# Optimization experiments

Measured on AMD Instinct MI355X. Metric: run time of the kernel, lower is better.

The kernel has to match this reference:

```python
import jax, jax.numpy as jnp
import numpy as np

CENTER = 7          # center_size
K = 5               # neighbourhood_size
DIL = 1             # dilation
EPS_LN = 1e-5       # torch F.layer_norm default eps
EPS_COS = 1e-8      # torch F.cosine_similarity default eps


def _unfold_image(image, k):
    """torch F.unfold(image, k, stride=1, padding=k//2) -> [B, T, C*k*k]."""
    B, C, H, W = image.shape
    p = k // 2
    padded = jnp.pad(image, ((0, 0), (0, 0), (p, p), (p, p)))
    # channel-major patch layout (c, ki, kj), matching torch.unfold
    patches = jnp.stack([padded[:, :, i:i + H, j:j + W]
                         for i in range(k) for j in range(k)], axis=2)  # [B,C,k*k,H,W]
    return patches.reshape(B, C * k * k, H * W).transpose(0, 2, 1)       # [B,T,D]


def _neighbour_indices(H, W, k, dil):
    """generate_local_indices with constant padding value N=H*W, center removed -> [T, k*k-1]."""
    half = (k - 1) // 2 * dil
    N = H * W
    inds = np.arange(N).reshape(H, W)
    padded = np.full((H + 2 * half, W + 2 * half), N, dtype=np.int64)
    padded[half:half + H, half:half + W] = inds
    cols = [padded[i * dil:i * dil + H, j * dil:j * dil + W].reshape(-1)
            for i in range(k) for j in range(k)]
    local = np.stack(cols, axis=-1)  # [T, k*k]
    center = (k * k) // 2
    keep = [s for s in range(k * k) if s != center]
    return jnp.asarray(local[:, keep])  # [T, S], S = k*k-1


def setup_inputs() -> dict:
    key = jax.random.key(0)
    image = jax.random.uniform(key, (2, 3, 128, 128), dtype=jnp.float32)
    return {"image": image}


def reference(image):
    B, C, H, W = image.shape
    T = H * W
    kc = CENTER

    # im2col of center patches: [B, T, C*kc*kc]
    bu = _unfold_image(image, kc)

    # per-channel LayerNorm over kc*kc elements (no affine), then +1.0 twice
    bu = bu.reshape(B, T, C, kc * kc)
    mu = bu.mean(axis=-1, keepdims=True)
    var = ((bu - mu) ** 2).mean(axis=-1, keepdims=True)
    bu = (bu - mu) / jnp.sqrt(var + EPS_LN)
    bu = bu.reshape(B, T, C * kc * kc) + 2.0  # [B,T,D]

    # local neighbourhood indices (padding index == T marks out-of-bounds)
    nb = _neighbour_indices(H, W, K, DIL)  # [T, S]

    # gather surround patches; row T is the invalid (zero) row
    bu_ext = jnp.concatenate([bu, jnp.zeros((B, 1, bu.shape[-1]), bu.dtype)], axis=1)
    surround = bu_ext[:, nb]  # [B,T,S,D]

    # cosine similarity between each center patch and its S neighbours
    dot = jnp.einsum('btd,btsd->bts', bu, surround)
    n_node = jnp.linalg.norm(bu, axis=-1)        # [B,T]
    n_sur = jnp.linalg.norm(surround, axis=-1)   # [B,T,S]
    cos = dot / jnp.maximum(n_node[:, :, None] * n_sur, EPS_COS)
    dist = (1.0 - cos) * 0.5  # = 1 - (1+cos)/2

    # masked mean over valid neighbours
    mask = (nb != T).astype(dist.dtype)  # [T,S]
    sal = (dist * mask).sum(-1) / mask.sum(-1)
    return sal.reshape(B, H, W)
```

## Files before the change

### kernel.cpp

```cpp
#include <hip/hip_runtime.h>

#define HH 128
#define WW 128
#define TX 8
#define TY 8
#define IR 22
#define ISTR 23
#define S4 16
#define S4S 17
#define S2 12
#define S2S 13
#define NTHR 256

__global__ void __launch_bounds__(NTHR)
err_kernel(const float* __restrict__ img, float* __restrict__ out) {
    __shared__ float s_img[3][IR][ISTR];
    __shared__ union U1 {
        float rs[2][3][IR][S4S];
        float H[36][18][S2];
    } u1;
    __shared__ float s_mu[3][S4][S4S];
    __shared__ float s_r [3][S4][S4S];
    __shared__ union U2 {
        float nsq[3][S2][S2S];
        float part[12][S2][S2S];
    } u2;
    __shared__ float s_rnrm[S2][S2S];

    const int tid = threadIdx.x;
    const int x0 = blockIdx.x * TX, y0 = blockIdx.y * TY;
    const float* imgb = img + (size_t)blockIdx.z * 3 * HH * WW;

    for (int i = tid; i < 3 * IR * IR; i += NTHR) {
        const int c = i / (IR * IR);
        const int rem = i - c * IR * IR;
        const int iy = rem / IR, ix = rem - iy * IR;
        const int yy = y0 - 7 + iy, xx = x0 - 7 + ix;
        float v = 0.f;
        if ((unsigned)yy < HH && (unsigned)xx < WW)
            v = imgb[c * HH * WW + yy * WW + xx];
        s_img[c][iy][ix] = v;
    }
    __syncthreads();

    if (tid < 66) {
        const int c = tid / 22, row = tid - c * 22;
        float f[22];
#pragma unroll
        for (int j = 0; j < 22; ++j) f[j] = s_img[c][row][j];
        float s = 0.f, s2 = 0.f;
#pragma unroll
        for (int k = 0; k < 7; ++k) { s += f[k]; s2 = fmaf(f[k], f[k], s2); }
        u1.rs[0][c][row][0] = s; u1.rs[1][c][row][0] = s2;
#pragma unroll
        for (int x = 1; x < S4; ++x) {
            s += f[x + 6] - f[x - 1];
            s2 += fmaf(f[x + 6], f[x + 6], -f[x - 1] * f[x - 1]);
            u1.rs[0][c][row][x] = s; u1.rs[1][c][row][x] = s2;
        }
    }
    __syncthreads();

    if (tid < 96) {
        const int c = tid / 32;
        const int rem = tid - c * 32;
        const int col = rem >> 1, h = rem & 1;
        const int r0 = h * 8;
        float s = 0.f, s2 = 0.f;
#pragma unroll
        for (int k = 0; k < 7; ++k) { s += u1.rs[0][c][r0 + k][col]; s2 += u1.rs[1][c][r0 + k][col]; }
#pragma unroll
        for (int i = 0; i < 8; ++i) {
            const int rr4 = r0 + i;
            const float mu  = s * (1.f / 49.f);
            const float var = fmaxf(fmaf(-mu, mu, s2 * (1.f / 49.f)), 0.f);
            const float rv  = rsqrtf(var + 1e-5f);
            s_mu[c][rr4][col] = mu;
            s_r [c][rr4][col] = rv;
            const int sr = rr4 - 2, sc = col - 2;
            if ((unsigned)sr < S2 && (unsigned)sc < S2)
                u2.nsq[c][sr][sc] = fmaf(49.f * var, rv * rv, 196.f);
            if (i < 7) {
                s  += u1.rs[0][c][rr4 + 7][col] - u1.rs[0][c][rr4][col];
                s2 += u1.rs[1][c][rr4 + 7][col] - u1.rs[1][c][rr4][col];
            }
        }
    }
    __syncthreads();

    if (tid < 144) {
        const int py = tid / 12, px = tid - py * 12;
        s_rnrm[py][px] = rsqrtf(u2.nsq[0][py][px] + u2.nsq[1][py][px] + u2.nsq[2][py][px]);
    }
    for (int q = tid; q < 648; q += NTHR) {
        const int cd = q / 18;
        const int prow = q - cd * 18;
        const int dI = cd / 3, c = cd - dI * 3;
        const int u = dI + 13;
        const int dy = u / 5 - 2, dx = u - (u / 5) * 5 - 2;
        const float* rowA = &s_img[c][prow + 2][2];
        const float* rowB = &s_img[c][prow + 2 + dy][2 + dx];
        float P[18];
#pragma unroll
        for (int j = 0; j < 18; ++j) P[j] = rowA[j] * rowB[j];
        float hsum = P[0] + P[1] + P[2] + P[3] + P[4] + P[5] + P[6];
        u1.H[cd][prow][0] = hsum;
#pragma unroll
        for (int j = 1; j < S2; ++j) { hsum += P[j + 6] - P[j - 1]; u1.H[cd][prow][j] = hsum; }
    }
    __syncthreads();

    if (tid < 144) {
        const int dI = tid / 12, col = tid - dI * 12;
        const int u = dI + 13;
        const int dy = u / 5 - 2, dx = u - (u / 5) * 5 - 2;
        float B[3];
#pragma unroll
        for (int c = 0; c < 3; ++c) {
            float b = 0.f;
#pragma unroll
            for (int k = 0; k < 7; ++k) b += u1.H[dI * 3 + c][k][col];
            B[c] = b;
        }
#pragma unroll
        for (int y = 0; y < S2; ++y) {
            float acc = 0.f;
#pragma unroll
            for (int c = 0; c < 3; ++c) {
                const float m = s_mu[c][y + 2][col + 2] * s_mu[c][y + 2 + dy][col + 2 + dx];
                const float v = fmaf(-49.f, m, B[c]);
                acc = fmaf(v, s_r[c][y + 2][col + 2] * s_r[c][y + 2 + dy][col + 2 + dx], acc);
            }
            u2.part[dI][y][col] = acc;
            if (y < S2 - 1) {
#pragma unroll
                for (int c = 0; c < 3; ++c)
                    B[c] += u1.H[dI * 3 + c][y + 7][col] - u1.H[dI * 3 + c][y][col];
            }
        }
    }
    __syncthreads();

    if (tid < 64) {
        const int ty = tid >> 3, tx = tid & 7;
        const int gy = y0 + ty, gx = x0 + tx;
        const float rnt = s_rnrm[ty + 2][tx + 2];
        float acc = 0.f, cnt = 0.f;
#pragma unroll
        for (int dI = 0; dI < 12; ++dI) {
            const int u = dI + 13;
            const int dy = u / 5 - 2, dx = u - (u / 5) * 5 - 2;
            if ((unsigned)(gy + dy) < HH && (unsigned)(gx + dx) < WW) {
                const float ps = u2.part[dI][ty + 2][tx + 2];
                acc = fmaf(588.f + ps, s_rnrm[ty + 2 + dy][tx + 2 + dx], acc);
                cnt += 1.f;
            }
            if ((unsigned)(gy - dy) < HH && (unsigned)(gx - dx) < WW) {
                const float ps = u2.part[dI][ty + 2 - dy][tx + 2 - dx];
                acc = fmaf(588.f + ps, s_rnrm[ty + 2 - dy][tx + 2 - dx], acc);
                cnt += 1.f;
            }
        }
        out[(size_t)blockIdx.z * HH * WW + gy * WW + gx] = 0.5f - acc * rnt / (2.f * cnt);
    }
}

extern "C" void kernel_launch(void* const* d_in, const int* in_sizes, int n_in,
                              void* d_out, int out_size, void* d_ws, size_t ws_size,
                              hipStream_t stream) {
    const float* img = (const float*)d_in[0];
    float* out = (float*)d_out;
    dim3 grid(WW / TX, HH / TY, 2);
    dim3 block(NTHR);
    hipLaunchKernelGGL(err_kernel, grid, block, 0, stream, img, out);
}
```

Measured before the change: 14.38 us.

## Vectorize shared-memory access and regroup product-row work by vertical offset

Pads the image tile row stride to 28 so rows can be read with float4 loads. Merges per-channel mean and rstd into one interleaved stat array holding rv and mu*rv, so the neighbour pass fetches them with float4 loads. The horizontal product-sum stage now assigns one thread per (dy, channel, row), reusing loaded row pairs across several dx offsets and writing results with float4 stores. The vertical sweep preloads all 18 H values per channel into registers. This cuts LDS instruction count and per-thread index arithmetic, at the cost of higher register pressure and uneven per-thread work (2 versus 5 offsets).

```diff
diff --git a/kernel.cpp b/kernel.cpp
--- a/kernel.cpp
+++ b/kernel.cpp
@@ -5,36 +5,31 @@
 #define TX 8
 #define TY 8
 #define IR 22
-#define ISTR 23
-#define S4 16
-#define S4S 17
-#define S2 12
-#define S2S 13
+#define ISTR 28
 #define NTHR 256
 
 __global__ void __launch_bounds__(NTHR)
 err_kernel(const float* __restrict__ img, float* __restrict__ out) {
     __shared__ float s_img[3][IR][ISTR];
     __shared__ union U1 {
-        float rs[2][3][IR][S4S];
-        float H[36][18][S2];
+        float rs[2][3][IR][17];
+        float H[36][18][12];
     } u1;
-    __shared__ float s_mu[3][S4][S4S];
-    __shared__ float s_r [3][S4][S4S];
+    __shared__ float s_stat[16][16][8];
     __shared__ union U2 {
-        float nsq[3][S2][S2S];
-        float part[12][S2][S2S];
+        float nsq[3][12][12];
+        float part[12][12][12];
     } u2;
-    __shared__ float s_rnrm[S2][S2S];
+    __shared__ float s_rnrm[12][12];
 
     const int tid = threadIdx.x;
     const int x0 = blockIdx.x * TX, y0 = blockIdx.y * TY;
     const float* imgb = img + (size_t)blockIdx.z * 3 * HH * WW;
 
-    for (int i = tid; i < 3 * IR * IR; i += NTHR) {
-        const int c = i / (IR * IR);
-        const int rem = i - c * IR * IR;
-        const int iy = rem / IR, ix = rem - iy * IR;
+    for (int i = tid; i < 3 * IR * ISTR; i += NTHR) {
+        const int c = i / (IR * ISTR);
+        const int rem = i - c * IR * ISTR;
+        const int iy = rem / ISTR, ix = rem - iy * ISTR;
         const int yy = y0 - 7 + iy, xx = x0 - 7 + ix;
         float v = 0.f;
         if ((unsigned)yy < HH && (unsigned)xx < WW)
@@ -45,15 +40,16 @@
 
     if (tid < 66) {
         const int c = tid / 22, row = tid - c * 22;
-        float f[22];
+        float f[24];
+        const float4* rp = (const float4*)&s_img[c][row][0];
 #pragma unroll
-        for (int j = 0; j < 22; ++j) f[j] = s_img[c][row][j];
+        for (int q = 0; q < 6; ++q) ((float4*)f)[q] = rp[q];
         float s = 0.f, s2 = 0.f;
 #pragma unroll
         for (int k = 0; k < 7; ++k) { s += f[k]; s2 = fmaf(f[k], f[k], s2); }
         u1.rs[0][c][row][0] = s; u1.rs[1][c][row][0] = s2;
 #pragma unroll
-        for (int x = 1; x < S4; ++x) {
+        for (int x = 1; x < 16; ++x) {
             s += f[x + 6] - f[x - 1];
             s2 += fmaf(f[x + 6], f[x + 6], -f[x - 1] * f[x - 1]);
             u1.rs[0][c][row][x] = s; u1.rs[1][c][row][x] = s2;
@@ -64,8 +60,8 @@
     if (tid < 96) {
         const int c = tid / 32;
         const int rem = tid - c * 32;
-        const int col = rem >> 1, h = rem & 1;
-        const int r0 = h * 8;
+        const int col = rem >> 1, h2 = rem & 1;
+        const int r0 = h2 * 8;
         float s = 0.f, s2 = 0.f;
 #pragma unroll
         for (int k = 0; k < 7; ++k) { s += u1.rs[0][c][r0 + k][col]; s2 += u1.rs[1][c][r0 + k][col]; }
@@ -75,10 +71,10 @@
             const float mu  = s * (1.f / 49.f);
             const float var = fmaxf(fmaf(-mu, mu, s2 * (1.f / 49.f)), 0.f);
             const float rv  = rsqrtf(var + 1e-5f);
-            s_mu[c][rr4][col] = mu;
-            s_r [c][rr4][col] = rv;
+            s_stat[rr4][col][c]     = rv;
+            s_stat[rr4][col][4 + c] = mu * rv;
             const int sr = rr4 - 2, sc = col - 2;
-            if ((unsigned)sr < S2 && (unsigned)sc < S2)
+            if ((unsigned)sr < 12 && (unsigned)sc < 12)
                 u2.nsq[c][sr][sc] = fmaf(49.f * var, rv * rv, 196.f);
             if (i < 7) {
                 s  += u1.rs[0][c][rr4 + 7][col] - u1.rs[0][c][rr4][col];
@@ -92,21 +88,35 @@
         const int py = tid / 12, px = tid - py * 12;
         s_rnrm[py][px] = rsqrtf(u2.nsq[0][py][px] + u2.nsq[1][py][px] + u2.nsq[2][py][px]);
     }
-    for (int q = tid; q < 648; q += NTHR) {
-        const int cd = q / 18;
-        const int prow = q - cd * 18;
-        const int dI = cd / 3, c = cd - dI * 3;
-        const int u = dI + 13;
-        const int dy = u / 5 - 2, dx = u - (u / 5) * 5 - 2;
-        const float* rowA = &s_img[c][prow + 2][2];
-        const float* rowB = &s_img[c][prow + 2 + dy][2 + dx];
-        float P[18];
+    if (tid < 162) {
+        const int dy = tid / 54;
+        const int rem = tid - dy * 54;
+        const int c = rem / 18, prow = rem - c * 18;
+        float rA[24], rB[24];
+        const float4* pA = (const float4*)&s_img[c][prow + 2][0];
+        const float4* pB = (const float4*)&s_img[c][prow + 2 + dy][0];
 #pragma unroll
-        for (int j = 0; j < 18; ++j) P[j] = rowA[j] * rowB[j];
-        float hsum = P[0] + P[1] + P[2] + P[3] + P[4] + P[5] + P[6];
-        u1.H[cd][prow][0] = hsum;
-#pragma unroll
-        for (int j = 1; j < S2; ++j) { hsum += P[j + 6] - P[j - 1]; u1.H[cd][prow][j] = hsum; }
+        for (int q = 0; q < 6; ++q) { ((float4*)rA)[q] = pA[q]; ((float4*)rB)[q] = pB[q]; }
+
+#define EMIT(dI, dx) do {                                                   \
+        float P[18];                                                        \
+        _Pragma("unroll")                                                   \
+        for (int j = 0; j < 18; ++j) P[j] = rA[j + 2] * rB[j + 2 + (dx)];   \
+        float w[12];                                                        \
+        float h = P[0]+P[1]+P[2]+P[3]+P[4]+P[5]+P[6];                       \
+        w[0] = h;                                                           \
+        _Pragma("unroll")                                                   \
+        for (int j = 1; j < 12; ++j) { h += P[j + 6] - P[j - 1]; w[j] = h; }\
+        float4* wp = (float4*)&u1.H[(dI) * 3 + c][prow][0];                 \
+        wp[0] = make_float4(w[0], w[1], w[2],  w[3]);                       \
+        wp[1] = make_float4(w[4], w[5], w[6],  w[7]);                       \
+        wp[2] = make_float4(w[8], w[9], w[10], w[11]);                      \
+    } while (0)
+
+        if (dy == 0)      { EMIT(0, 1); EMIT(1, 2); }
+        else if (dy == 1) { EMIT(2, -2); EMIT(3, -1); EMIT(4, 0); EMIT(5, 1); EMIT(6, 2); }
+        else              { EMIT(7, -2); EMIT(8, -1); EMIT(9, 0); EMIT(10, 1); EMIT(11, 2); }
+#undef EMIT
     }
     __syncthreads();
 
@@ -114,28 +124,27 @@
         const int dI = tid / 12, col = tid - dI * 12;
         const int u = dI + 13;
         const int dy = u / 5 - 2, dx = u - (u / 5) * 5 - 2;
-        float B[3];
+        float h[3][18];
 #pragma unroll
-        for (int c = 0; c < 3; ++c) {
-            float b = 0.f;
+        for (int c = 0; c < 3; ++c)
 #pragma unroll
-            for (int k = 0; k < 7; ++k) b += u1.H[dI * 3 + c][k][col];
-            B[c] = b;
-        }
+            for (int k = 0; k < 18; ++k) h[c][k] = u1.H[dI * 3 + c][k][col];
+        float B0 = h[0][0]+h[0][1]+h[0][2]+h[0][3]+h[0][4]+h[0][5]+h[0][6];
+        float B1 = h[1][0]+h[1][1]+h[1][2]+h[1][3]+h[1][4]+h[1][5]+h[1][6];
+        float B2 = h[2][0]+h[2][1]+h[2][2]+h[2][3]+h[2][4]+h[2][5]+h[2][6];
 #pragma unroll
-        for (int y = 0; y < S2; ++y) {
-            float acc = 0.f;
-#pragma unroll
-            for (int c = 0; c < 3; ++c) {
-                const float m = s_mu[c][y + 2][col + 2] * s_mu[c][y + 2 + dy][col + 2 + dx];
-                const float v = fmaf(-49.f, m, B[c]);
-                acc = fmaf(v, s_r[c][y + 2][col + 2] * s_r[c][y + 2 + dy][col + 2 + dx], acc);
-            }
-            u2.part[dI][y][col] = acc;
-            if (y < S2 - 1) {
-#pragma unroll
-                for (int c = 0; c < 3; ++c)
-                    B[c] += u1.H[dI * 3 + c][y + 7][col] - u1.H[dI * 3 + c][y][col];
+        for (int y = 0; y < 12; ++y) {
+            const float4 t1 = *(const float4*)&s_stat[y + 2][col + 2][0];
+            const float4 t2 = *(const float4*)&s_stat[y + 2][col + 2][4];
+            const float4 n1 = *(const float4*)&s_stat[y + 2 + dy][col + 2 + dx][0];
+            const float4 n2 = *(const float4*)&s_stat[y + 2 + dy][col + 2 + dx][4];
+            float acc = B0 * t1.x * n1.x + B1 * t1.y * n1.y + B2 * t1.z * n1.z;
+            float ma  = t2.x * n2.x + t2.y * n2.y + t2.z * n2.z;
+            u2.part[dI][y][col] = fmaf(-49.f, ma, acc);
+            if (y < 11) {
+                B0 += h[0][y + 7] - h[0][y];
+                B1 += h[1][y + 7] - h[1][y];
+                B2 += h[2][y + 7] - h[2][y];
             }
         }
     }
@@ -151,13 +160,13 @@
             const int u = dI + 13;
             const int dy = u / 5 - 2, dx = u - (u / 5) * 5 - 2;
             if ((unsigned)(gy + dy) < HH && (unsigned)(gx + dx) < WW) {
-                const float ps = u2.part[dI][ty + 2][tx + 2];
-                acc = fmaf(588.f + ps, s_rnrm[ty + 2 + dy][tx + 2 + dx], acc);
+                acc = fmaf(588.f + u2.part[dI][ty + 2][tx + 2],
+                           s_rnrm[ty + 2 + dy][tx + 2 + dx], acc);
                 cnt += 1.f;
             }
             if ((unsigned)(gy - dy) < HH && (unsigned)(gx - dx) < WW) {
-                const float ps = u2.part[dI][ty + 2 - dy][tx + 2 - dx];
-                acc = fmaf(588.f + ps, s_rnrm[ty + 2 - dy][tx + 2 - dx], acc);
+                acc = fmaf(588.f + u2.part[dI][ty + 2 - dy][tx + 2 - dx],
+                           s_rnrm[ty + 2 - dy][tx + 2 - dx], acc);
                 cnt += 1.f;
             }
         }
```

After: 14.37 us. No clear change (-0.1%).
